# Optimization experiments

Hardware: AMD Instinct MI355X
Metric: run time of the kernel (lower is better)

## Reference

```python
import jax, jax.numpy as jnp
import numpy as np

B, T, D, H = 2, 2048, 1024, 16
DK = D // H  # 64, head dim (even, required by RoPE pairing)


def setup_inputs() -> dict:
    key = jax.random.key(0)
    ks = jax.random.split(key, 9)
    sc = 1.0 / np.sqrt(D)
    x = jax.random.normal(ks[0], (B, T, D), jnp.float32)
    wq = jax.random.normal(ks[1], (D, D), jnp.float32) * sc
    bq = jax.random.normal(ks[2], (D,), jnp.float32) * 0.01
    wk = jax.random.normal(ks[3], (D, D), jnp.float32) * sc
    bk = jax.random.normal(ks[4], (D,), jnp.float32) * 0.01
    wv = jax.random.normal(ks[5], (D, D), jnp.float32) * sc
    bv = jax.random.normal(ks[6], (D,), jnp.float32) * 0.01
    wo = jax.random.normal(ks[7], (D, D), jnp.float32) * sc
    bo = jax.random.normal(ks[8], (D,), jnp.float32) * 0.01
    # causal mask, True = masked (matches masked_fill semantics); dim==3 -> broadcast over heads
    attn_mask = jnp.triu(jnp.ones((T, T), dtype=bool), 1)[None]  # [1,T,T]
    return dict(x=x, wq=wq, bq=bq, wk=wk, bk=bk, wv=wv, bv=bv, wo=wo, bo=bo,
                attn_mask=attn_mask)


def _rope(xh, sin, cos):
    # xh: [B,H,T,DK]; sin/cos: [T,DK/2]
    x1 = xh[..., 0::2]
    x2 = xh[..., 1::2]
    return jnp.stack([x1 * cos - x2 * sin, x1 * sin + x2 * cos], axis=-1).reshape(xh.shape)


def reference(x, wq, bq, wk, bk, wv, bv, wo, bo, attn_mask):
    q = (x @ wq.T + bq).reshape(B, T, H, DK).transpose(0, 2, 1, 3)  # [B,H,T,DK]
    k = (x @ wk.T + bk).reshape(B, T, H, DK).transpose(0, 2, 1, 3)
    v = (x @ wv.T + bv).reshape(B, T, H, DK).transpose(0, 2, 1, 3)
    # RoPE (seq_offset = 0)
    theta = 10000.0 ** (jnp.arange(0, DK, 2, dtype=jnp.float32) / DK)  # [DK/2]
    pos = jnp.arange(T, dtype=jnp.float32)[:, None]                    # [T,1]
    ang = pos / theta                                                  # [T,DK/2]
    sin, cos = jnp.sin(ang), jnp.cos(ang)
    q = _rope(q, sin, cos)
    k = _rope(k, sin, cos)
    # fp32 stable attention (inputs already fp32)
    scores = jnp.einsum('bhtd,bhsd->bhts', q, k) / np.sqrt(DK)
    scores = jnp.where(attn_mask[:, None], -1e9, scores)  # mask broadcast over heads
    attn = jax.nn.softmax(scores, axis=-1)
    ctx = jnp.einsum('bhts,bhsd->bhtd', attn, v)
    ctx = ctx.transpose(0, 2, 1, 3).reshape(B, T, D)
    return ctx @ wo.T + bo
```

## Files before the change

### kernel.cpp

```cpp
#include <hip/hip_runtime.h>
#include <stdint.h>
#include <stddef.h>

#define T_ 2048
#define D_ 1024
#define H_ 16

typedef __attribute__((ext_vector_type(8))) short short8;
typedef __attribute__((ext_vector_type(4))) float f32x4;
typedef __attribute__((ext_vector_type(4))) short s16x4;

__device__ __forceinline__ unsigned short f2bf(float f){
  union { float f; unsigned u; } c; c.f = f;
  unsigned u = c.u;
  return (unsigned short)((u + 0x7fffu + ((u >> 16) & 1u)) >> 16);
}

__device__ __forceinline__ unsigned pk_bf16(float lo, float hi){
  unsigned r;
  asm("v_cvt_pk_bf16_f32 %0, %1, %2" : "=v"(r) : "v"(lo), "v"(hi));
  return r;
}

__device__ __forceinline__ float fexp2(float x){
#if __has_builtin(__builtin_amdgcn_exp2f)
  return __builtin_amdgcn_exp2f(x);
#else
  return exp2f(x);
#endif
}

__device__ __forceinline__ f32x4 mfma16(short8 a, short8 b, f32x4 c){
  return __builtin_amdgcn_mfma_f32_16x16x32_bf16(a, b, c, 0, 0, 0);
}

__device__ __forceinline__ void gload16(const void* g, void* l){
  __builtin_amdgcn_global_load_lds(
      (const __attribute__((address_space(1))) unsigned*)g,
      (__attribute__((address_space(3))) unsigned*)l, 16, 0, 0);
}

__global__ __launch_bounds__(256) void k_prep(const float* __restrict__ x,
    const float* __restrict__ wq, const float* __restrict__ wk,
    const float* __restrict__ wv, const float* __restrict__ wo,
    unsigned short* __restrict__ xb, unsigned short* __restrict__ wqkv,
    unsigned short* __restrict__ wob)
{
  const long long NX = 4194304LL, NW = 1048576LL;
  long long base = ((long long)blockIdx.x * 256 + threadIdx.x) * 4;
  const float* s; unsigned short* d;
  if (base < NX){ s = x + base; d = xb + base; }
  else if (base < NX + 3*NW){
    long long j = base - NX;
    if (j < NW) s = wq + j;
    else if (j < 2*NW) s = wk + (j - NW);
    else s = wv + (j - 2*NW);
    d = wqkv + j;
  } else if (base < NX + 4*NW){
    long long j = base - NX - 3*NW;
    s = wo + j; d = wob + j;
  } else return;
  float4 v = *(const float4*)s;
  d[0] = f2bf(v.x); d[1] = f2bf(v.y); d[2] = f2bf(v.z); d[3] = f2bf(v.w);
}

__global__ __launch_bounds__(256) void k_rope(float* __restrict__ tab){
  int i = blockIdx.x * 256 + threadIdx.x;
  if (i >= T_ * 32) return;
  int t = i >> 5, p = i & 31;
  float ang = (float)t * powf(10000.0f, -(float)p * (1.0f / 32.0f));
  tab[i] = sinf(ang);
  tab[T_ * 32 + i] = cosf(ang);
}

__device__ __forceinline__ void gemm_core(const unsigned short* __restrict__ A,
    const unsigned short* __restrict__ Bm, int m0, int n0,
    unsigned short* lA, unsigned short* lB, f32x4 (&acc)[4][4])
{
  const int tid = threadIdx.x, lane = tid & 63, wave = tid >> 6;
  const int wr = wave >> 1, wc = wave & 1;
  for (int mi = 0; mi < 4; ++mi)
    for (int ni = 0; ni < 4; ++ni)
      acc[mi][ni] = (f32x4){0.f, 0.f, 0.f, 0.f};
  for (int k0 = 0; k0 < 1024; k0 += 64){
    __syncthreads();
#pragma unroll
    for (int p = 0; p < 4; ++p){
      int c = p * 256 + tid, r = c >> 3, s = c & 7;
      int gs = (s ^ (r & 7)) << 3;
      gload16(A + (size_t)(m0 + r) * 1024 + k0 + gs, lA + c * 8);
      gload16(Bm + (size_t)(n0 + r) * 1024 + k0 + gs, lB + c * 8);
    }
    __syncthreads();
#pragma unroll
    for (int kk = 0; kk < 2; ++kk){
      int kslot = kk * 4 + (lane >> 4);
      short8 af[4], bf[4];
#pragma unroll
      for (int mi = 0; mi < 4; ++mi){
        int row = wr * 64 + mi * 16 + (lane & 15);
        af[mi] = *(const short8*)(lA + row * 64 + ((kslot ^ (row & 7)) << 3));
      }
#pragma unroll
      for (int ni = 0; ni < 4; ++ni){
        int row = wc * 64 + ni * 16 + (lane & 15);
        bf[ni] = *(const short8*)(lB + row * 64 + ((kslot ^ (row & 7)) << 3));
      }
#pragma unroll
      for (int mi = 0; mi < 4; ++mi)
#pragma unroll
        for (int ni = 0; ni < 4; ++ni)
          acc[mi][ni] = mfma16(af[mi], bf[ni], acc[mi][ni]);
    }
  }
}

__global__ __launch_bounds__(256) void k_qkv(const unsigned short* __restrict__ xb,
    const unsigned short* __restrict__ wqkv,
    const float* __restrict__ bq, const float* __restrict__ bk, const float* __restrict__ bv,
    const float* __restrict__ tab,
    unsigned short* __restrict__ Qw, unsigned short* __restrict__ Kw,
    unsigned short* __restrict__ Vw)
{
  __shared__ alignas(16) unsigned short lA[128 * 64];
  __shared__ alignas(16) unsigned short lB[128 * 64];
  int m0 = blockIdx.y * 128, n0 = blockIdx.x * 128;
  f32x4 acc[4][4];
  gemm_core(xb, wqkv, m0, n0, lA, lB, acc);
  int lane = threadIdx.x & 63, wave = threadIdx.x >> 6;
  int wr = wave >> 1, wc = wave & 1;
  int mat = n0 >> 10;
  const float* bias = (mat == 0) ? bq : (mat == 1 ? bk : bv);
  const float* st = tab; const float* ct = tab + T_ * 32;
  if (mat < 2){
    unsigned short* Out = (mat == 0) ? Qw : Kw;
    float qs = (mat == 0) ? 0.18033688011116f : 1.0f;
    for (int mi = 0; mi < 4; ++mi){
      for (int ni = 0; ni < 4; ++ni){
        int col = n0 + wc * 64 + ni * 16 + (lane & 15);
        int nn = col & 1023, h = nn >> 6, dd = nn & 63;
        float bsv = bias[nn];
        f32x4 v4 = acc[mi][ni];
#pragma unroll
        for (int r = 0; r < 4; ++r){
          int m = m0 + wr * 64 + mi * 16 + ((lane >> 4) << 2) + r;
          int bb = m >> 11, t = m & 2047;
          float v = v4[r] + bsv;
          float u = __shfl_xor(v, 1);
          int p = dd >> 1;
          float sv = st[t * 32 + p], cv = ct[t * 32 + p];
          float res = (dd & 1) ? (u * sv + v * cv) : (v * cv - u * sv);
          Out[((size_t)(bb * H_ + h) * T_ + t) * 64 + dd] = f2bf(res * qs);
        }
      }
    }
  } else {
    for (int mi = 0; mi < 4; ++mi){
      for (int ni = 0; ni < 4; ++ni){
        int col = n0 + wc * 64 + ni * 16 + (lane & 15);
        int nn = col & 1023, h = nn >> 6, dd = nn & 63;
        float bsv = bias[nn];
        int mb = m0 + wr * 64 + mi * 16 + ((lane >> 4) << 2);
        int bb = mb >> 11, t = mb & 2047;
        f32x4 v4 = acc[mi][ni];
        s16x4 o;
#pragma unroll
        for (int r = 0; r < 4; ++r) o[r] = (short)f2bf(v4[r] + bsv);
        *(s16x4*)(Vw + ((size_t)((bb * H_ + h) * 64 + dd)) * T_ + t) = o;
      }
    }
  }
}

__global__ __launch_bounds__(256) void k_attn(const unsigned short* __restrict__ Qw,
    const unsigned short* __restrict__ Kw, const unsigned short* __restrict__ Vt_g,
    unsigned short* __restrict__ ctxb)
{
  __shared__ alignas(16) unsigned short Kl[64 * 64];
  __shared__ alignas(16) unsigned short Vl[64 * 64];
  int qt = (int)gridDim.y - 1 - (int)blockIdx.y;
  int bh = blockIdx.x;
  int tid = threadIdx.x, lane = tid & 63, wave = tid >> 6;
  const unsigned short* Qb = Qw + (size_t)bh * T_ * 64;
  const unsigned short* Kb = Kw + (size_t)bh * T_ * 64;
  const unsigned short* Vb = Vt_g + (size_t)bh * 64 * T_;
  int q0 = qt * 128 + wave * 32;

  short8 qf[2][2];
#pragma unroll
  for (int mi = 0; mi < 2; ++mi){
    const unsigned short* qp = Qb + (size_t)(q0 + mi * 16 + (lane & 15)) * 64 + ((lane >> 4) << 3);
    qf[mi][0] = *(const short8*)qp;
    qf[mi][1] = *(const short8*)(qp + 32);
  }
  float mr[2] = {-1e30f, -1e30f}, lr[2] = {0.f, 0.f};
  f32x4 acc_o[2][4];
#pragma unroll
  for (int mi = 0; mi < 2; ++mi)
#pragma unroll
    for (int df = 0; df < 4; ++df) acc_o[mi][df] = (f32x4){0.f, 0.f, 0.f, 0.f};

  const int src0 = ((lane >> 4) & 1) * 32 + (lane & 15);
  const int src1 = src0 + 16;
  const bool hiHalf = lane >= 32;

  int ntiles = 2 * qt + 2;
  for (int jt = 0; jt < ntiles; ++jt){
    int j0 = jt * 64;
    __syncthreads();
#pragma unroll
    for (int p = 0; p < 2; ++p){
      int c = p * 256 + tid, r = c >> 3, s = c & 7;
      int gs = (s ^ (r & 7)) << 3;
      gload16(Kb + (size_t)(j0 + r) * 64 + gs, Kl + c * 8);
      gload16(Vb + (size_t)r * T_ + j0 + gs, Vl + c * 8);
    }
    __syncthreads();
    if (j0 > q0 + 31) continue;
    bool need_mask = (j0 + 63 > q0);

    f32x4 accs[2][4];
#pragma unroll
    for (int mi = 0; mi < 2; ++mi)
#pragma unroll
      for (int jf = 0; jf < 4; ++jf) accs[mi][jf] = (f32x4){0.f, 0.f, 0.f, 0.f};
#pragma unroll
    for (int kk = 0; kk < 2; ++kk){
      int kslot = kk * 4 + (lane >> 4);
      short8 kf[4];
#pragma unroll
      for (int jf = 0; jf < 4; ++jf){
        int row = jf * 16 + (lane & 15);
        kf[jf] = *(const short8*)(Kl + row * 64 + ((kslot ^ (row & 7)) << 3));
      }
#pragma unroll
      for (int mi = 0; mi < 2; ++mi)
#pragma unroll
        for (int jf = 0; jf < 4; ++jf)
          accs[mi][jf] = mfma16(kf[jf], qf[mi][kk], accs[mi][jf]);
    }

    unsigned w0[2][4], w1[2][4];
#pragma unroll
    for (int mi = 0; mi < 2; ++mi){
      int qa = q0 + mi * 16 + (lane & 15);
      float s[4][4];
      float mx = -1e30f;
#pragma unroll
      for (int jf = 0; jf < 4; ++jf)
#pragma unroll
        for (int r = 0; r < 4; ++r){
          float sv = accs[mi][jf][r];
          if (need_mask){
            int ja = j0 + jf * 16 + ((lane >> 4) << 2) + r;
            if (ja > qa) sv = -1e30f;
          }
          s[jf][r] = sv;
          mx = fmaxf(mx, sv);
        }
      mx = fmaxf(mx, __shfl_xor(mx, 16));
      mx = fmaxf(mx, __shfl_xor(mx, 32));
      float mn = fmaxf(mr[mi], mx);
      float sc = fexp2(mr[mi] - mn);
      mr[mi] = mn;
      float rs = 0.f;
#pragma unroll
      for (int jf = 0; jf < 4; ++jf)
#pragma unroll
        for (int r = 0; r < 4; ++r){
          float pe = fexp2(s[jf][r] - mn);
          s[jf][r] = pe;
          rs += pe;
        }
      rs += __shfl_xor(rs, 16);
      rs += __shfl_xor(rs, 32);
      lr[mi] = lr[mi] * sc + rs;
#pragma unroll
      for (int df = 0; df < 4; ++df){
        f32x4 a = acc_o[mi][df];
        a[0] *= sc; a[1] *= sc; a[2] *= sc; a[3] *= sc;
        acc_o[mi][df] = a;
      }
#pragma unroll
      for (int jf = 0; jf < 4; ++jf){
        w0[mi][jf] = pk_bf16(s[jf][0], s[jf][1]);
        w1[mi][jf] = pk_bf16(s[jf][2], s[jf][3]);
      }
    }

#pragma unroll
    for (int kk = 0; kk < 2; ++kk){
      int jslot = kk * 4 + (lane >> 4);
      short8 vf[4];
#pragma unroll
      for (int df = 0; df < 4; ++df){
        int row = df * 16 + (lane & 15);
        vf[df] = *(const short8*)(Vl + row * 64 + ((jslot ^ (row & 7)) << 3));
      }
#pragma unroll
      for (int mi = 0; mi < 2; ++mi){
        unsigned lo0 = (unsigned)__shfl((int)w0[mi][2*kk],   src0);
        unsigned hi0 = (unsigned)__shfl((int)w0[mi][2*kk+1], src0);
        unsigned lo1 = (unsigned)__shfl((int)w1[mi][2*kk],   src0);
        unsigned hi1 = (unsigned)__shfl((int)w1[mi][2*kk+1], src0);
        unsigned lo2 = (unsigned)__shfl((int)w0[mi][2*kk],   src1);
        unsigned hi2 = (unsigned)__shfl((int)w0[mi][2*kk+1], src1);
        unsigned lo3 = (unsigned)__shfl((int)w1[mi][2*kk],   src1);
        unsigned hi3 = (unsigned)__shfl((int)w1[mi][2*kk+1], src1);
        union { unsigned u[4]; short8 v; } pb;
        pb.u[0] = hiHalf ? hi0 : lo0;
        pb.u[1] = hiHalf ? hi1 : lo1;
        pb.u[2] = hiHalf ? hi2 : lo2;
        pb.u[3] = hiHalf ? hi3 : lo3;
#pragma unroll
        for (int df = 0; df < 4; ++df)
          acc_o[mi][df] = mfma16(vf[df], pb.v, acc_o[mi][df]);
      }
    }
  }

  int bb = bh >> 4, h = bh & 15;
#pragma unroll
  for (int mi = 0; mi < 2; ++mi){
    float inv = 1.0f / lr[mi];
    int t = q0 + mi * 16 + (lane & 15);
#pragma unroll
    for (int df = 0; df < 4; ++df){
      int d0 = df * 16 + ((lane >> 4) << 2);
      f32x4 a = acc_o[mi][df];
      s16x4 o;
#pragma unroll
      for (int r = 0; r < 4; ++r) o[r] = (short)f2bf(a[r] * inv);
      *(s16x4*)(ctxb + ((size_t)(bb * T_ + t)) * 1024 + h * 64 + d0) = o;
    }
  }
}

__global__ __launch_bounds__(256) void k_oproj(const unsigned short* __restrict__ ctxb,
    const unsigned short* __restrict__ wob, const float* __restrict__ bo,
    float* __restrict__ out)
{
  __shared__ alignas(16) unsigned short lA[128 * 64];
  __shared__ alignas(16) unsigned short lB[128 * 64];
  int m0 = blockIdx.y * 128, n0 = blockIdx.x * 128;
  f32x4 acc[4][4];
  gemm_core(ctxb, wob, m0, n0, lA, lB, acc);
  int lane = threadIdx.x & 63, wave = threadIdx.x >> 6;
  int wr = wave >> 1, wc = wave & 1;
  for (int mi = 0; mi < 4; ++mi)
    for (int ni = 0; ni < 4; ++ni){
      int col = n0 + wc * 64 + ni * 16 + (lane & 15);
      float bsv = bo[col];
      f32x4 v4 = acc[mi][ni];
#pragma unroll
      for (int r = 0; r < 4; ++r){
        int m = m0 + wr * 64 + mi * 16 + ((lane >> 4) << 2) + r;
        out[(size_t)m * 1024 + col] = v4[r] + bsv;
      }
    }
}

extern "C" void kernel_launch(void* const* d_in, const int* in_sizes, int n_in,
                              void* d_out, int out_size, void* d_ws, size_t ws_size,
                              hipStream_t stream)
{
  const float* x  = (const float*)d_in[0];
  const float* wq = (const float*)d_in[1];
  const float* bq = (const float*)d_in[2];
  const float* wk = (const float*)d_in[3];
  const float* bk = (const float*)d_in[4];
  const float* wv = (const float*)d_in[5];
  const float* bv = (const float*)d_in[6];
  const float* wo = (const float*)d_in[7];
  const float* bo = (const float*)d_in[8];
  char* w = (char*)d_ws;
  unsigned short* xb   = (unsigned short*)(w);
  unsigned short* wqkv = (unsigned short*)(w + (8 << 20));
  unsigned short* wob  = (unsigned short*)(w + (14 << 20));
  unsigned short* Qw   = (unsigned short*)(w + (16 << 20));
  unsigned short* Kw   = (unsigned short*)(w + (24 << 20));
  unsigned short* Vw   = (unsigned short*)(w + (32 << 20));
  unsigned short* ctxb = (unsigned short*)(w + (40 << 20));
  float* tab           = (float*)(w + (48 << 20));

  k_prep<<<8192, 256, 0, stream>>>(x, wq, wk, wv, wo, xb, wqkv, wob);
  k_rope<<<256, 256, 0, stream>>>(tab);
  k_qkv<<<dim3(24, 32), 256, 0, stream>>>(xb, wqkv, bq, bk, bv, tab, Qw, Kw, Vw);
  k_attn<<<dim3(32, 16), 256, 0, stream>>>(Qw, Kw, Vw, ctxb);
  k_oproj<<<dim3(8, 32), 256, 0, stream>>>(ctxb, wob, bo, (float*)d_out);
}
```

Measured before the change: 148.4 us.

## Retile attention to 64-query blocks with 128-key tiles, lazy rescale, fuse RoPE table

Attention blocks now cover 64 queries (16 per wave) instead of 128, while each K/V tile grows from 64 to 128 keys. The grid becomes a 1-D launch of 1024 blocks with a swizzled mapping from block id to head and query tile, and launch bounds ask for 4 blocks per CU. The online softmax only rescales the accumulator when the running max grows by more than 8 (log2 units), so most tiles skip the rescale. The RoPE table is now built inside the prep kernel, which removes one launch. In exchange, each wave reuses its K/V tile across fewer queries and more blocks are scheduled, and the lazy rescale relies on the score range staying bounded to avoid overflow.

```diff
diff --git a/kernel.cpp b/kernel.cpp
--- a/kernel.cpp
+++ b/kernel.cpp
@@ -44,8 +44,15 @@
     const float* __restrict__ wq, const float* __restrict__ wk,
     const float* __restrict__ wv, const float* __restrict__ wo,
     unsigned short* __restrict__ xb, unsigned short* __restrict__ wqkv,
-    unsigned short* __restrict__ wob)
-{
+    unsigned short* __restrict__ wob, float* __restrict__ tab)
+{
+  if (blockIdx.x < 256){
+    int i = blockIdx.x * 256 + threadIdx.x;
+    int t = i >> 5, p = i & 31;
+    float ang = (float)t * powf(10000.0f, -(float)p * (1.0f / 32.0f));
+    tab[i] = sinf(ang);
+    tab[T_ * 32 + i] = cosf(ang);
+  }
   const long long NX = 4194304LL, NW = 1048576LL;
   long long base = ((long long)blockIdx.x * 256 + threadIdx.x) * 4;
   const float* s; unsigned short* d;
@@ -62,15 +69,6 @@
   } else return;
   float4 v = *(const float4*)s;
   d[0] = f2bf(v.x); d[1] = f2bf(v.y); d[2] = f2bf(v.z); d[3] = f2bf(v.w);
-}
-
-__global__ __launch_bounds__(256) void k_rope(float* __restrict__ tab){
-  int i = blockIdx.x * 256 + threadIdx.x;
-  if (i >= T_ * 32) return;
-  int t = i >> 5, p = i & 31;
-  float ang = (float)t * powf(10000.0f, -(float)p * (1.0f / 32.0f));
-  tab[i] = sinf(ang);
-  tab[T_ * 32 + i] = cosf(ang);
 }
 
 __device__ __forceinline__ void gemm_core(const unsigned short* __restrict__ A,
@@ -172,85 +170,82 @@
   }
 }
 
-__global__ __launch_bounds__(256) void k_attn(const unsigned short* __restrict__ Qw,
+__global__ __launch_bounds__(256, 4) void k_attn(const unsigned short* __restrict__ Qw,
     const unsigned short* __restrict__ Kw, const unsigned short* __restrict__ Vt_g,
     unsigned short* __restrict__ ctxb)
 {
-  __shared__ alignas(16) unsigned short Kl[64 * 64];
-  __shared__ alignas(16) unsigned short Vl[64 * 64];
-  int qt = (int)gridDim.y - 1 - (int)blockIdx.y;
-  int bh = blockIdx.x;
+  __shared__ alignas(16) unsigned short Kl[128 * 64];
+  __shared__ alignas(16) unsigned short Vl[64 * 128];
+  int bid = blockIdx.x;
+  int swz = (bid & 7) * 128 + (bid >> 3);
+  int bh = swz >> 5;
+  int qt = 31 - (swz & 31);
   int tid = threadIdx.x, lane = tid & 63, wave = tid >> 6;
   const unsigned short* Qb = Qw + (size_t)bh * T_ * 64;
   const unsigned short* Kb = Kw + (size_t)bh * T_ * 64;
   const unsigned short* Vb = Vt_g + (size_t)bh * 64 * T_;
-  int q0 = qt * 128 + wave * 32;
-
-  short8 qf[2][2];
-#pragma unroll
-  for (int mi = 0; mi < 2; ++mi){
-    const unsigned short* qp = Qb + (size_t)(q0 + mi * 16 + (lane & 15)) * 64 + ((lane >> 4) << 3);
-    qf[mi][0] = *(const short8*)qp;
-    qf[mi][1] = *(const short8*)(qp + 32);
-  }
-  float mr[2] = {-1e30f, -1e30f}, lr[2] = {0.f, 0.f};
-  f32x4 acc_o[2][4];
-#pragma unroll
-  for (int mi = 0; mi < 2; ++mi)
-#pragma unroll
-    for (int df = 0; df < 4; ++df) acc_o[mi][df] = (f32x4){0.f, 0.f, 0.f, 0.f};
+  int q0 = qt * 64 + wave * 16;
+
+  short8 qf[2];
+  {
+    const unsigned short* qp = Qb + (size_t)(q0 + (lane & 15)) * 64 + ((lane >> 4) << 3);
+    qf[0] = *(const short8*)qp;
+    qf[1] = *(const short8*)(qp + 32);
+  }
+  float mr = -1e30f, lr = 0.f;
+  f32x4 acc_o[4];
+#pragma unroll
+  for (int df = 0; df < 4; ++df) acc_o[df] = (f32x4){0.f, 0.f, 0.f, 0.f};
 
   const int src0 = ((lane >> 4) & 1) * 32 + (lane & 15);
   const int src1 = src0 + 16;
   const bool hiHalf = lane >= 32;
-
-  int ntiles = 2 * qt + 2;
+  int ntiles = (qt >> 1) + 1;
+
   for (int jt = 0; jt < ntiles; ++jt){
-    int j0 = jt * 64;
+    int j0 = jt * 128;
     __syncthreads();
 #pragma unroll
-    for (int p = 0; p < 2; ++p){
+    for (int p = 0; p < 4; ++p){
       int c = p * 256 + tid, r = c >> 3, s = c & 7;
-      int gs = (s ^ (r & 7)) << 3;
-      gload16(Kb + (size_t)(j0 + r) * 64 + gs, Kl + c * 8);
-      gload16(Vb + (size_t)r * T_ + j0 + gs, Vl + c * 8);
+      gload16(Kb + (size_t)(j0 + r) * 64 + ((s ^ (r & 7)) << 3), Kl + c * 8);
+    }
+#pragma unroll
+    for (int p = 0; p < 4; ++p){
+      int c = p * 256 + tid, r = c >> 4, s = c & 15;
+      gload16(Vb + (size_t)r * T_ + j0 + ((s ^ (r & 7)) << 3), Vl + c * 8);
     }
     __syncthreads();
-    if (j0 > q0 + 31) continue;
-    bool need_mask = (j0 + 63 > q0);
-
-    f32x4 accs[2][4];
-#pragma unroll
-    for (int mi = 0; mi < 2; ++mi)
-#pragma unroll
-      for (int jf = 0; jf < 4; ++jf) accs[mi][jf] = (f32x4){0.f, 0.f, 0.f, 0.f};
+    if (j0 > q0 + 15) continue;
+    bool need_mask = (j0 + 127 > q0);
+
+    f32x4 accs[8];
+#pragma unroll
+    for (int jf = 0; jf < 8; ++jf) accs[jf] = (f32x4){0.f, 0.f, 0.f, 0.f};
 #pragma unroll
     for (int kk = 0; kk < 2; ++kk){
       int kslot = kk * 4 + (lane >> 4);
-      short8 kf[4];
-#pragma unroll
-      for (int jf = 0; jf < 4; ++jf){
+      short8 kf[8];
+#pragma unroll
+      for (int jf = 0; jf < 8; ++jf){
         int row = jf * 16 + (lane & 15);
         kf[jf] = *(const short8*)(Kl + row * 64 + ((kslot ^ (row & 7)) << 3));
       }
 #pragma unroll
-      for (int mi = 0; mi < 2; ++mi)
-#pragma unroll
-        for (int jf = 0; jf < 4; ++jf)
-          accs[mi][jf] = mfma16(kf[jf], qf[mi][kk], accs[mi][jf]);
-    }
-
-    unsigned w0[2][4], w1[2][4];
-#pragma unroll
-    for (int mi = 0; mi < 2; ++mi){
-      int qa = q0 + mi * 16 + (lane & 15);
-      float s[4][4];
+      for (int jf = 0; jf < 8; ++jf)
+        accs[jf] = mfma16(kf[jf], qf[kk], accs[jf]);
+    }
+
+    unsigned w0[8], w1[8];
+    {
+      int qa = q0 + (lane & 15);
+      float s[8][4];
       float mx = -1e30f;
 #pragma unroll
-      for (int jf = 0; jf < 4; ++jf)
+      for (int jf = 0; jf < 8; ++jf)
 #pragma unroll
         for (int r = 0; r < 4; ++r){
-          float sv = accs[mi][jf][r];
+          float sv = accs[jf][r];
           if (need_mask){
             int ja = j0 + jf * 16 + ((lane >> 4) << 2) + r;
             if (ja > qa) sv = -1e30f;
@@ -260,12 +255,22 @@
         }
       mx = fmaxf(mx, __shfl_xor(mx, 16));
       mx = fmaxf(mx, __shfl_xor(mx, 32));
-      float mn = fmaxf(mr[mi], mx);
-      float sc = fexp2(mr[mi] - mn);
-      mr[mi] = mn;
+      float mn = mr;
+      if (!__all(mx <= mn + 8.0f)){
+        mn = fmaxf(mn, mx);
+        float sc = fexp2(mr - mn);
+        mr = mn;
+        lr *= sc;
+#pragma unroll
+        for (int df = 0; df < 4; ++df){
+          f32x4 a = acc_o[df];
+          a[0] *= sc; a[1] *= sc; a[2] *= sc; a[3] *= sc;
+          acc_o[df] = a;
+        }
+      }
       float rs = 0.f;
 #pragma unroll
-      for (int jf = 0; jf < 4; ++jf)
+      for (int jf = 0; jf < 8; ++jf)
 #pragma unroll
         for (int r = 0; r < 4; ++r){
           float pe = fexp2(s[jf][r] - mn);
@@ -274,60 +279,50 @@
         }
       rs += __shfl_xor(rs, 16);
       rs += __shfl_xor(rs, 32);
-      lr[mi] = lr[mi] * sc + rs;
-#pragma unroll
-      for (int df = 0; df < 4; ++df){
-        f32x4 a = acc_o[mi][df];
-        a[0] *= sc; a[1] *= sc; a[2] *= sc; a[3] *= sc;
-        acc_o[mi][df] = a;
-      }
-#pragma unroll
-      for (int jf = 0; jf < 4; ++jf){
-        w0[mi][jf] = pk_bf16(s[jf][0], s[jf][1]);
-        w1[mi][jf] = pk_bf16(s[jf][2], s[jf][3]);
-      }
-    }
-
-#pragma unroll
-    for (int kk = 0; kk < 2; ++kk){
+      lr += rs;
+#pragma unroll
+      for (int jf = 0; jf < 8; ++jf){
+        w0[jf] = pk_bf16(s[jf][0], s[jf][1]);
+        w1[jf] = pk_bf16(s[jf][2], s[jf][3]);
+      }
+    }
+
+#pragma unroll
+    for (int kk = 0; kk < 4; ++kk){
       int jslot = kk * 4 + (lane >> 4);
       short8 vf[4];
 #pragma unroll
       for (int df = 0; df < 4; ++df){
         int row = df * 16 + (lane & 15);
-        vf[df] = *(const short8*)(Vl + row * 64 + ((jslot ^ (row & 7)) << 3));
-      }
-#pragma unroll
-      for (int mi = 0; mi < 2; ++mi){
-        unsigned lo0 = (unsigned)__shfl((int)w0[mi][2*kk],   src0);
-        unsigned hi0 = (unsigned)__shfl((int)w0[mi][2*kk+1], src0);
-        unsigned lo1 = (unsigned)__shfl((int)w1[mi][2*kk],   src0);
-        unsigned hi1 = (unsigned)__shfl((int)w1[mi][2*kk+1], src0);
-        unsigned lo2 = (unsigned)__shfl((int)w0[mi][2*kk],   src1);
-        unsigned hi2 = (unsigned)__shfl((int)w0[mi][2*kk+1], src1);
-        unsigned lo3 = (unsigned)__shfl((int)w1[mi][2*kk],   src1);
-        unsigned hi3 = (unsigned)__shfl((int)w1[mi][2*kk+1], src1);
-        union { unsigned u[4]; short8 v; } pb;
-        pb.u[0] = hiHalf ? hi0 : lo0;
-        pb.u[1] = hiHalf ? hi1 : lo1;
-        pb.u[2] = hiHalf ? hi2 : lo2;
-        pb.u[3] = hiHalf ? hi3 : lo3;
-#pragma unroll
-        for (int df = 0; df < 4; ++df)
-          acc_o[mi][df] = mfma16(vf[df], pb.v, acc_o[mi][df]);
-      }
+        vf[df] = *(const short8*)(Vl + row * 128 + ((jslot ^ (row & 7)) << 3));
+      }
+      unsigned lo0 = (unsigned)__shfl((int)w0[2*kk],   src0);
+      unsigned hi0 = (unsigned)__shfl((int)w0[2*kk+1], src0);
+      unsigned lo1 = (unsigned)__shfl((int)w1[2*kk],   src0);
+      unsigned hi1 = (unsigned)__shfl((int)w1[2*kk+1], src0);
+      unsigned lo2 = (unsigned)__shfl((int)w0[2*kk],   src1);
+      unsigned hi2 = (unsigned)__shfl((int)w0[2*kk+1], src1);
+      unsigned lo3 = (unsigned)__shfl((int)w1[2*kk],   src1);
+      unsigned hi3 = (unsigned)__shfl((int)w1[2*kk+1], src1);
+      union { unsigned u[4]; short8 v; } pb;
+      pb.u[0] = hiHalf ? hi0 : lo0;
+      pb.u[1] = hiHalf ? hi1 : lo1;
+      pb.u[2] = hiHalf ? hi2 : lo2;
+      pb.u[3] = hiHalf ? hi3 : lo3;
+#pragma unroll
+      for (int df = 0; df < 4; ++df)
+        acc_o[df] = mfma16(vf[df], pb.v, acc_o[df]);
     }
   }
 
   int bb = bh >> 4, h = bh & 15;
-#pragma unroll
-  for (int mi = 0; mi < 2; ++mi){
-    float inv = 1.0f / lr[mi];
-    int t = q0 + mi * 16 + (lane & 15);
+  {
+    float inv = 1.0f / lr;
+    int t = q0 + (lane & 15);
 #pragma unroll
     for (int df = 0; df < 4; ++df){
       int d0 = df * 16 + ((lane >> 4) << 2);
-      f32x4 a = acc_o[mi][df];
+      f32x4 a = acc_o[df];
       s16x4 o;
 #pragma unroll
       for (int r = 0; r < 4; ++r) o[r] = (short)f2bf(a[r] * inv);
@@ -383,9 +378,8 @@
   unsigned short* ctxb = (unsigned short*)(w + (40 << 20));
   float* tab           = (float*)(w + (48 << 20));
 
-  k_prep<<<8192, 256, 0, stream>>>(x, wq, wk, wv, wo, xb, wqkv, wob);
-  k_rope<<<256, 256, 0, stream>>>(tab);
+  k_prep<<<8192, 256, 0, stream>>>(x, wq, wk, wv, wo, xb, wqkv, wob, tab);
   k_qkv<<<dim3(24, 32), 256, 0, stream>>>(xb, wqkv, bq, bk, bv, tab, Qw, Kw, Vw);
-  k_attn<<<dim3(32, 16), 256, 0, stream>>>(Qw, Kw, Vw, ctxb);
+  k_attn<<<1024, 256, 0, stream>>>(Qw, Kw, Vw, ctxb);
   k_oproj<<<dim3(8, 32), 256, 0, stream>>>(ctxb, wob, bo, (float*)d_out);
 }
```

Result: slower. 157.4 us (+6.1%).

## Fuse RoPE table into prep, vectorize bf16 conversion, enlarge attention KV tile

Applied to the files above, without the earlier changes.

Folds the RoPE sin/cos table generation into the prep kernel, which removes one launch. The prep kernel now converts 8 floats per thread with packed bf16 stores instead of 4 scalar stores. The attention kernel processes 128-key tiles instead of 64, which halves the number of barrier-separated load/compute iterations. The larger tile doubles LDS use and the score registers per wave, which may lower occupancy. It also wastes more masked work on diagonal tiles.

```diff
diff --git a/kernel.cpp b/kernel.cpp
--- a/kernel.cpp
+++ b/kernel.cpp
@@ -44,10 +44,17 @@
     const float* __restrict__ wq, const float* __restrict__ wk,
     const float* __restrict__ wv, const float* __restrict__ wo,
     unsigned short* __restrict__ xb, unsigned short* __restrict__ wqkv,
-    unsigned short* __restrict__ wob)
-{
+    unsigned short* __restrict__ wob, float* __restrict__ tab)
+{
+  if (blockIdx.x < 256){
+    int i = blockIdx.x * 256 + threadIdx.x;
+    int t = i >> 5, p = i & 31;
+    float ang = (float)t * powf(10000.0f, -(float)p * (1.0f / 32.0f));
+    tab[i] = sinf(ang);
+    tab[T_ * 32 + i] = cosf(ang);
+  }
   const long long NX = 4194304LL, NW = 1048576LL;
-  long long base = ((long long)blockIdx.x * 256 + threadIdx.x) * 4;
+  long long base = ((long long)blockIdx.x * 256 + threadIdx.x) * 8;
   const float* s; unsigned short* d;
   if (base < NX){ s = x + base; d = xb + base; }
   else if (base < NX + 3*NW){
@@ -60,17 +67,14 @@
     long long j = base - NX - 3*NW;
     s = wo + j; d = wob + j;
   } else return;
-  float4 v = *(const float4*)s;
-  d[0] = f2bf(v.x); d[1] = f2bf(v.y); d[2] = f2bf(v.z); d[3] = f2bf(v.w);
-}
-
-__global__ __launch_bounds__(256) void k_rope(float* __restrict__ tab){
-  int i = blockIdx.x * 256 + threadIdx.x;
-  if (i >= T_ * 32) return;
-  int t = i >> 5, p = i & 31;
-  float ang = (float)t * powf(10000.0f, -(float)p * (1.0f / 32.0f));
-  tab[i] = sinf(ang);
-  tab[T_ * 32 + i] = cosf(ang);
+  float4 a = *(const float4*)s;
+  float4 b = *(const float4*)(s + 4);
+  union { unsigned u[4]; short8 v; } o;
+  o.u[0] = pk_bf16(a.x, a.y);
+  o.u[1] = pk_bf16(a.z, a.w);
+  o.u[2] = pk_bf16(b.x, b.y);
+  o.u[3] = pk_bf16(b.z, b.w);
+  *(short8*)d = o.v;
 }
 
 __device__ __forceinline__ void gemm_core(const unsigned short* __restrict__ A,
@@ -176,8 +180,8 @@
     const unsigned short* __restrict__ Kw, const unsigned short* __restrict__ Vt_g,
     unsigned short* __restrict__ ctxb)
 {
-  __shared__ alignas(16) unsigned short Kl[64 * 64];
-  __shared__ alignas(16) unsigned short Vl[64 * 64];
+  __shared__ alignas(16) unsigned short Kl[128 * 64];
+  __shared__ alignas(16) unsigned short Vl[64 * 128];
   int qt = (int)gridDim.y - 1 - (int)blockIdx.y;
   int bh = blockIdx.x;
   int tid = threadIdx.x, lane = tid & 63, wave = tid >> 6;
@@ -204,50 +208,52 @@
   const int src1 = src0 + 16;
   const bool hiHalf = lane >= 32;
 
-  int ntiles = 2 * qt + 2;
+  int ntiles = qt + 1;
   for (int jt = 0; jt < ntiles; ++jt){
-    int j0 = jt * 64;
+    int j0 = jt * 128;
     __syncthreads();
 #pragma unroll
-    for (int p = 0; p < 2; ++p){
+    for (int p = 0; p < 4; ++p){
       int c = p * 256 + tid, r = c >> 3, s = c & 7;
-      int gs = (s ^ (r & 7)) << 3;
-      gload16(Kb + (size_t)(j0 + r) * 64 + gs, Kl + c * 8);
-      gload16(Vb + (size_t)r * T_ + j0 + gs, Vl + c * 8);
+      gload16(Kb + (size_t)(j0 + r) * 64 + ((s ^ (r & 7)) << 3), Kl + c * 8);
+    }
+#pragma unroll
+    for (int p = 0; p < 4; ++p){
+      int c = p * 256 + tid, r = c >> 4, s = c & 15;
+      gload16(Vb + (size_t)r * T_ + j0 + ((s ^ (r & 7)) << 3), Vl + c * 8);
     }
     __syncthreads();
     if (j0 > q0 + 31) continue;
-    bool need_mask = (j0 + 63 > q0);
-
-    f32x4 accs[2][4];
+    bool need_mask = (j0 + 127 > q0);
+
+    f32x4 accs[2][8];
 #pragma unroll
     for (int mi = 0; mi < 2; ++mi)
 #pragma unroll
-      for (int jf = 0; jf < 4; ++jf) accs[mi][jf] = (f32x4){0.f, 0.f, 0.f, 0.f};
+      for (int jf = 0; jf < 8; ++jf) accs[mi][jf] = (f32x4){0.f, 0.f, 0.f, 0.f};
 #pragma unroll
     for (int kk = 0; kk < 2; ++kk){
       int kslot = kk * 4 + (lane >> 4);
-      short8 kf[4];
-#pragma unroll
-      for (int jf = 0; jf < 4; ++jf){
+      short8 kf[8];
+#pragma unroll
+      for (int jf = 0; jf < 8; ++jf){
         int row = jf * 16 + (lane & 15);
         kf[jf] = *(const short8*)(Kl + row * 64 + ((kslot ^ (row & 7)) << 3));
       }
 #pragma unroll
       for (int mi = 0; mi < 2; ++mi)
 #pragma unroll
-        for (int jf = 0; jf < 4; ++jf)
+        for (int jf = 0; jf < 8; ++jf)
           accs[mi][jf] = mfma16(kf[jf], qf[mi][kk], accs[mi][jf]);
     }
 
-    unsigned w0[2][4], w1[2][4];
+    unsigned w0[2][8], w1[2][8];
 #pragma unroll
     for (int mi = 0; mi < 2; ++mi){
       int qa = q0 + mi * 16 + (lane & 15);
-      float s[4][4];
       float mx = -1e30f;
 #pragma unroll
-      for (int jf = 0; jf < 4; ++jf)
+      for (int jf = 0; jf < 8; ++jf)
 #pragma unroll
         for (int r = 0; r < 4; ++r){
           float sv = accs[mi][jf][r];
@@ -255,7 +261,7 @@
             int ja = j0 + jf * 16 + ((lane >> 4) << 2) + r;
             if (ja > qa) sv = -1e30f;
           }
-          s[jf][r] = sv;
+          accs[mi][jf][r] = sv;
           mx = fmaxf(mx, sv);
         }
       mx = fmaxf(mx, __shfl_xor(mx, 16));
@@ -265,11 +271,11 @@
       mr[mi] = mn;
       float rs = 0.f;
 #pragma unroll
-      for (int jf = 0; jf < 4; ++jf)
+      for (int jf = 0; jf < 8; ++jf)
 #pragma unroll
         for (int r = 0; r < 4; ++r){
-          float pe = fexp2(s[jf][r] - mn);
-          s[jf][r] = pe;
+          float pe = fexp2(accs[mi][jf][r] - mn);
+          accs[mi][jf][r] = pe;
           rs += pe;
         }
       rs += __shfl_xor(rs, 16);
@@ -282,20 +288,20 @@
         acc_o[mi][df] = a;
       }
 #pragma unroll
-      for (int jf = 0; jf < 4; ++jf){
-        w0[mi][jf] = pk_bf16(s[jf][0], s[jf][1]);
-        w1[mi][jf] = pk_bf16(s[jf][2], s[jf][3]);
-      }
-    }
-
-#pragma unroll
-    for (int kk = 0; kk < 2; ++kk){
+      for (int jf = 0; jf < 8; ++jf){
+        w0[mi][jf] = pk_bf16(accs[mi][jf][0], accs[mi][jf][1]);
+        w1[mi][jf] = pk_bf16(accs[mi][jf][2], accs[mi][jf][3]);
+      }
+    }
+
+#pragma unroll
+    for (int kk = 0; kk < 4; ++kk){
       int jslot = kk * 4 + (lane >> 4);
       short8 vf[4];
 #pragma unroll
       for (int df = 0; df < 4; ++df){
         int row = df * 16 + (lane & 15);
-        vf[df] = *(const short8*)(Vl + row * 64 + ((jslot ^ (row & 7)) << 3));
+        vf[df] = *(const short8*)(Vl + row * 128 + ((jslot ^ (row & 7)) << 3));
       }
 #pragma unroll
       for (int mi = 0; mi < 2; ++mi){
@@ -383,8 +389,7 @@
   unsigned short* ctxb = (unsigned short*)(w + (40 << 20));
   float* tab           = (float*)(w + (48 << 20));
 
-  k_prep<<<8192, 256, 0, stream>>>(x, wq, wk, wv, wo, xb, wqkv, wob);
-  k_rope<<<256, 256, 0, stream>>>(tab);
+  k_prep<<<4096, 256, 0, stream>>>(x, wq, wk, wv, wo, xb, wqkv, wob, tab);
   k_qkv<<<dim3(24, 32), 256, 0, stream>>>(xb, wqkv, bq, bk, bv, tab, Qw, Kw, Vw);
   k_attn<<<dim3(32, 16), 256, 0, stream>>>(Qw, Kw, Vw, ctxb);
   k_oproj<<<dim3(8, 32), 256, 0, stream>>>(ctxb, wob, bo, (float*)d_out);
```

After: 141.0 us. -5.0%, faster.
